# Kernel tuning notes

Hardware: AMD Instinct MI355X
Metric: run time of the kernel (lower is better)

Reference implementation:

```python
import jax, jax.numpy as jnp
import numpy as np

B = 1048576  # number of Gaussians
EPS = 1e-8


def setup_inputs() -> dict:
    key = jax.random.key(0)
    ks = jax.random.split(key, 6)
    return {
        "loc1": jax.random.normal(ks[0], (B, 3), dtype=jnp.float32),
        "scale1": jax.random.uniform(ks[1], (B, 3), dtype=jnp.float32),
        "rot_matrix1": jax.random.normal(ks[2], (B, 3, 3), dtype=jnp.float32),
        "loc2": jax.random.normal(ks[3], (B, 3), dtype=jnp.float32),
        "scale2": jax.random.uniform(ks[4], (B, 3), dtype=jnp.float32),
        "rot_matrix2": jax.random.normal(ks[5], (B, 3, 3), dtype=jnp.float32),
    }


def reference(loc1, scale1, rot_matrix1, loc2, scale2, rot_matrix2):
    # Wasserstein-2 distance between batched 3D Gaussians.
    scale1 = jnp.clip(scale1, EPS)
    scale2 = jnp.clip(scale2, EPS)

    loc_diff2 = jnp.sum((loc1 - loc2) ** 2, axis=-1)  # [B]

    # cov2 = R2 diag(scale2) R2^T  -> [B,3,3]
    cov2 = jnp.einsum('bij,bj,bkj->bik', rot_matrix2, scale2, rot_matrix2)

    # cov2 rotated into frame 1: R1^T cov2 R1
    cov2_R1 = jnp.einsum('bji,bjk,bkl->bil', rot_matrix1, cov2, rot_matrix1)

    # E = diag(sqrt(scale1)) cov2_R1 diag(sqrt(scale1)), symmetrized
    s1_sqrt = jnp.sqrt(scale1)  # [B,3]
    E = s1_sqrt[:, :, None] * cov2_R1 * s1_sqrt[:, None, :]
    E = 0.5 * (E + jnp.swapaxes(E, -1, -2)) + EPS * jnp.eye(3, dtype=E.dtype)

    eigs = jnp.clip(jnp.linalg.eigvalsh(E), EPS)  # [B,3]
    E_sqrt_trace = jnp.sqrt(eigs).sum(axis=-1)  # [B]

    cov_w = (scale1.sum(axis=-1)
             + jnp.einsum('bii->b', cov2)
             - 2.0 * E_sqrt_trace)
    cov_w = jnp.clip(cov_w, 0.0)

    return jnp.sqrt(jnp.clip(loc_diff2 + cov_w, EPS))
```

## Files before the change

### kernel.cpp

```cpp
#include <hip/hip_runtime.h>
#include <math.h>

#define EPSF 1e-8f

__device__ __forceinline__ float tr_sqrt_eig(double a00, double a11, double a22,
                                             double a01, double a02, double a12)
{
    double q = (a00 + a11 + a22) * (1.0 / 3.0);
    double b00 = a00 - q, b11 = a11 - q, b22 = a22 - q;
    double p1 = a01 * a01 + a02 * a02 + a12 * a12;
    double p2 = b00 * b00 + b11 * b11 + b22 * b22 + 2.0 * p1;

    if (p2 <= 1e-30) {
        return 3.0f * sqrtf(fmaxf((float)q, EPSF));
    }

    double x = p2 * (1.0 / 6.0);
    double inv = rsqrt(x);
    double p = x * inv;
    double detB = b00 * (b11 * b22 - a12 * a12)
                - a01 * (a01 * b22 - a12 * a02)
                + a02 * (a01 * a12 - b11 * a02);
    double r = 0.5 * detB * (inv * inv * inv);
    r = fmin(1.0, fmax(-1.0, r));

    float phi = acosf((float)r) * (1.0f / 3.0f);
    float qf = (float)q;
    float tp = 2.0f * (float)p;
    float e0 = qf + tp * cosf(phi);
    float e1 = qf + tp * cosf(phi - 2.0943951023931953f);
    float e2 = qf + tp * cosf(phi + 2.0943951023931953f);
    return sqrtf(fmaxf(e0, EPSF)) + sqrtf(fmaxf(e1, EPSF)) + sqrtf(fmaxf(e2, EPSF));
}

__global__ __launch_bounds__(64) void wasserstein_kernel(
    const float* __restrict__ loc1, const float* __restrict__ scale1,
    const float* __restrict__ rot1, const float* __restrict__ loc2,
    const float* __restrict__ scale2, const float* __restrict__ rot2,
    float* __restrict__ out, int B4)
{
    int t = blockIdx.x * blockDim.x + threadIdx.x;
    if (t >= B4) return;

    const float4* l1p = (const float4*)loc1   + 3 * t;
    const float4* l2p = (const float4*)loc2   + 3 * t;
    const float4* s1p = (const float4*)scale1 + 3 * t;
    const float4* s2p = (const float4*)scale2 + 3 * t;
    const float4* r1p = (const float4*)rot1   + 9 * t;
    const float4* r2p = (const float4*)rot2   + 9 * t;

    float loc_diff2[4];
    {
        float L1[12], L2[12];
#pragma unroll
        for (int k = 0; k < 3; k++) {
            float4 a = l1p[k], b = l2p[k];
            L1[4 * k + 0] = a.x; L1[4 * k + 1] = a.y; L1[4 * k + 2] = a.z; L1[4 * k + 3] = a.w;
            L2[4 * k + 0] = b.x; L2[4 * k + 1] = b.y; L2[4 * k + 2] = b.z; L2[4 * k + 3] = b.w;
        }
#pragma unroll
        for (int g = 0; g < 4; g++) {
            float d0 = L1[3 * g + 0] - L2[3 * g + 0];
            float d1 = L1[3 * g + 1] - L2[3 * g + 1];
            float d2 = L1[3 * g + 2] - L2[3 * g + 2];
            loc_diff2[g] = d0 * d0 + d1 * d1 + d2 * d2;
        }
    }

    float cov2[4][6];
    float tr_cov2[4];
    {
        float S2[12], R2[36];
#pragma unroll
        for (int k = 0; k < 3; k++) {
            float4 v = s2p[k];
            S2[4 * k + 0] = v.x; S2[4 * k + 1] = v.y; S2[4 * k + 2] = v.z; S2[4 * k + 3] = v.w;
        }
#pragma unroll
        for (int k = 0; k < 9; k++) {
            float4 v = r2p[k];
            R2[4 * k + 0] = v.x; R2[4 * k + 1] = v.y; R2[4 * k + 2] = v.z; R2[4 * k + 3] = v.w;
        }
#pragma unroll
        for (int g = 0; g < 4; g++) {
            float s0 = fmaxf(S2[3 * g + 0], EPSF);
            float s1 = fmaxf(S2[3 * g + 1], EPSF);
            float s2 = fmaxf(S2[3 * g + 2], EPSF);
            const float* R = R2 + 9 * g;
            float c00 = R[0] * s0 * R[0] + R[1] * s1 * R[1] + R[2] * s2 * R[2];
            float c11 = R[3] * s0 * R[3] + R[4] * s1 * R[4] + R[5] * s2 * R[5];
            float c22 = R[6] * s0 * R[6] + R[7] * s1 * R[7] + R[8] * s2 * R[8];
            float c01 = R[0] * s0 * R[3] + R[1] * s1 * R[4] + R[2] * s2 * R[5];
            float c02 = R[0] * s0 * R[6] + R[1] * s1 * R[7] + R[2] * s2 * R[8];
            float c12 = R[3] * s0 * R[6] + R[4] * s1 * R[7] + R[5] * s2 * R[8];
            cov2[g][0] = c00; cov2[g][1] = c11; cov2[g][2] = c22;
            cov2[g][3] = c01; cov2[g][4] = c02; cov2[g][5] = c12;
            tr_cov2[g] = c00 + c11 + c22;
        }
    }

    float res[4];
    {
        float S1[12], R1[36];
#pragma unroll
        for (int k = 0; k < 3; k++) {
            float4 v = s1p[k];
            S1[4 * k + 0] = v.x; S1[4 * k + 1] = v.y; S1[4 * k + 2] = v.z; S1[4 * k + 3] = v.w;
        }
#pragma unroll
        for (int k = 0; k < 9; k++) {
            float4 v = r1p[k];
            R1[4 * k + 0] = v.x; R1[4 * k + 1] = v.y; R1[4 * k + 2] = v.z; R1[4 * k + 3] = v.w;
        }
#pragma unroll
        for (int g = 0; g < 4; g++) {
            float s0 = fmaxf(S1[3 * g + 0], EPSF);
            float s1 = fmaxf(S1[3 * g + 1], EPSF);
            float s2 = fmaxf(S1[3 * g + 2], EPSF);
            const float* R = R1 + 9 * g;
            float C[3][3];
            C[0][0] = cov2[g][0]; C[1][1] = cov2[g][1]; C[2][2] = cov2[g][2];
            C[0][1] = C[1][0] = cov2[g][3];
            C[0][2] = C[2][0] = cov2[g][4];
            C[1][2] = C[2][1] = cov2[g][5];

            float T[3][3];
#pragma unroll
            for (int r = 0; r < 3; r++)
#pragma unroll
                for (int c = 0; c < 3; c++)
                    T[r][c] = C[r][0] * R[c] + C[r][1] * R[3 + c] + C[r][2] * R[6 + c];

            float M[3][3];
#pragma unroll
            for (int r = 0; r < 3; r++)
#pragma unroll
                for (int c = 0; c < 3; c++)
                    M[r][c] = R[r] * T[0][c] + R[3 + r] * T[1][c] + R[6 + r] * T[2][c];

            float ss0 = sqrtf(s0), ss1 = sqrtf(s1), ss2 = sqrtf(s2);
            double a00 = (double)(s0 * M[0][0]) + 1e-8;
            double a11 = (double)(s1 * M[1][1]) + 1e-8;
            double a22 = (double)(s2 * M[2][2]) + 1e-8;
            double a01 = (double)(0.5f * (M[0][1] + M[1][0]) * ss0 * ss1);
            double a02 = (double)(0.5f * (M[0][2] + M[2][0]) * ss0 * ss2);
            double a12 = (double)(0.5f * (M[1][2] + M[2][1]) * ss1 * ss2);

            float trs = tr_sqrt_eig(a00, a11, a22, a01, a02, a12);

            float cov_w = (s0 + s1 + s2) + tr_cov2[g] - 2.0f * trs;
            cov_w = fmaxf(cov_w, 0.0f);
            res[g] = sqrtf(fmaxf(loc_diff2[g] + cov_w, EPSF));
        }
    }

    float4 o;
    o.x = res[0]; o.y = res[1]; o.z = res[2]; o.w = res[3];
    ((float4*)out)[t] = o;
}

extern "C" void kernel_launch(void* const* d_in, const int* in_sizes, int n_in,
                              void* d_out, int out_size, void* d_ws, size_t ws_size,
                              hipStream_t stream) {
    const float* loc1   = (const float*)d_in[0];
    const float* scale1 = (const float*)d_in[1];
    const float* rot1   = (const float*)d_in[2];
    const float* loc2   = (const float*)d_in[3];
    const float* scale2 = (const float*)d_in[4];
    const float* rot2   = (const float*)d_in[5];
    float* out = (float*)d_out;

    int B = in_sizes[0] / 3;
    int B4 = B / 4;
    int block = 64;
    int grid = (B4 + block - 1) / block;
    wasserstein_kernel<<<grid, block, 0, stream>>>(loc1, scale1, rot1, loc2, scale2, rot2, out, B4);
}
```

Before: 160.5 us.

## Stage rotation matrices through LDS with coalesced loads, one Gaussian per thread

Switches from four Gaussians per thread with per-thread strided float4 loads to one Gaussian per thread in 256-thread blocks. The 3x3 rotation matrices are loaded cooperatively into shared memory with coalesced float4 accesses, then read back per thread. Locations and scales are read directly with scalar strided loads. This aims to improve global-memory coalescing and occupancy, at the cost of a block barrier, LDS traffic with stride-9 access, and no bounds check, which assumes B is a multiple of 256.

```diff
diff --git a/kernel.cpp b/kernel.cpp
--- a/kernel.cpp
+++ b/kernel.cpp
@@ -33,130 +33,93 @@
     return sqrtf(fmaxf(e0, EPSF)) + sqrtf(fmaxf(e1, EPSF)) + sqrtf(fmaxf(e2, EPSF));
 }
 
-__global__ __launch_bounds__(64) void wasserstein_kernel(
+__global__ __launch_bounds__(256) void wasserstein_kernel(
     const float* __restrict__ loc1, const float* __restrict__ scale1,
     const float* __restrict__ rot1, const float* __restrict__ loc2,
     const float* __restrict__ scale2, const float* __restrict__ rot2,
-    float* __restrict__ out, int B4)
+    float* __restrict__ out, int B)
 {
-    int t = blockIdx.x * blockDim.x + threadIdx.x;
-    if (t >= B4) return;
+    __shared__ float sR1[256 * 9];
+    __shared__ float sR2[256 * 9];
 
-    const float4* l1p = (const float4*)loc1   + 3 * t;
-    const float4* l2p = (const float4*)loc2   + 3 * t;
-    const float4* s1p = (const float4*)scale1 + 3 * t;
-    const float4* s2p = (const float4*)scale2 + 3 * t;
-    const float4* r1p = (const float4*)rot1   + 9 * t;
-    const float4* r2p = (const float4*)rot2   + 9 * t;
+    const int tid = threadIdx.x;
+    const int g = blockIdx.x * 256 + tid;
 
-    float loc_diff2[4];
     {
-        float L1[12], L2[12];
-#pragma unroll
-        for (int k = 0; k < 3; k++) {
-            float4 a = l1p[k], b = l2p[k];
-            L1[4 * k + 0] = a.x; L1[4 * k + 1] = a.y; L1[4 * k + 2] = a.z; L1[4 * k + 3] = a.w;
-            L2[4 * k + 0] = b.x; L2[4 * k + 1] = b.y; L2[4 * k + 2] = b.z; L2[4 * k + 3] = b.w;
-        }
-#pragma unroll
-        for (int g = 0; g < 4; g++) {
-            float d0 = L1[3 * g + 0] - L2[3 * g + 0];
-            float d1 = L1[3 * g + 1] - L2[3 * g + 1];
-            float d2 = L1[3 * g + 2] - L2[3 * g + 2];
-            loc_diff2[g] = d0 * d0 + d1 * d1 + d2 * d2;
+        const float4* r1g = (const float4*)rot1 + blockIdx.x * 576;
+        const float4* r2g = (const float4*)rot2 + blockIdx.x * 576;
+        float4* s1 = (float4*)sR1;
+        float4* s2 = (float4*)sR2;
+        s1[tid]       = r1g[tid];
+        s1[tid + 256] = r1g[tid + 256];
+        s2[tid]       = r2g[tid];
+        s2[tid + 256] = r2g[tid + 256];
+        if (tid < 64) {
+            s1[tid + 512] = r1g[tid + 512];
+            s2[tid + 512] = r2g[tid + 512];
         }
     }
 
-    float cov2[4][6];
-    float tr_cov2[4];
-    {
-        float S2[12], R2[36];
+    float a0 = loc1[3 * g], a1 = loc1[3 * g + 1], a2 = loc1[3 * g + 2];
+    float b0 = loc2[3 * g], b1 = loc2[3 * g + 1], b2 = loc2[3 * g + 2];
+    float s10 = fmaxf(scale1[3 * g], EPSF);
+    float s11 = fmaxf(scale1[3 * g + 1], EPSF);
+    float s12 = fmaxf(scale1[3 * g + 2], EPSF);
+    float s20 = fmaxf(scale2[3 * g], EPSF);
+    float s21 = fmaxf(scale2[3 * g + 1], EPSF);
+    float s22 = fmaxf(scale2[3 * g + 2], EPSF);
+
+    float d0 = a0 - b0, d1 = a1 - b1, d2 = a2 - b2;
+    float loc_diff2 = d0 * d0 + d1 * d1 + d2 * d2;
+
+    __syncthreads();
+
+    const float* R2 = sR2 + 9 * tid;
+    float R2r[9];
 #pragma unroll
-        for (int k = 0; k < 3; k++) {
-            float4 v = s2p[k];
-            S2[4 * k + 0] = v.x; S2[4 * k + 1] = v.y; S2[4 * k + 2] = v.z; S2[4 * k + 3] = v.w;
-        }
+    for (int k = 0; k < 9; k++) R2r[k] = R2[k];
+
+    float C[3][3];
+    C[0][0] = R2r[0] * s20 * R2r[0] + R2r[1] * s21 * R2r[1] + R2r[2] * s22 * R2r[2];
+    C[1][1] = R2r[3] * s20 * R2r[3] + R2r[4] * s21 * R2r[4] + R2r[5] * s22 * R2r[5];
+    C[2][2] = R2r[6] * s20 * R2r[6] + R2r[7] * s21 * R2r[7] + R2r[8] * s22 * R2r[8];
+    C[0][1] = C[1][0] = R2r[0] * s20 * R2r[3] + R2r[1] * s21 * R2r[4] + R2r[2] * s22 * R2r[5];
+    C[0][2] = C[2][0] = R2r[0] * s20 * R2r[6] + R2r[1] * s21 * R2r[7] + R2r[2] * s22 * R2r[8];
+    C[1][2] = C[2][1] = R2r[3] * s20 * R2r[6] + R2r[4] * s21 * R2r[7] + R2r[5] * s22 * R2r[8];
+    float tr_cov2 = C[0][0] + C[1][1] + C[2][2];
+
+    const float* R1 = sR1 + 9 * tid;
+    float R1r[9];
 #pragma unroll
-        for (int k = 0; k < 9; k++) {
-            float4 v = r2p[k];
-            R2[4 * k + 0] = v.x; R2[4 * k + 1] = v.y; R2[4 * k + 2] = v.z; R2[4 * k + 3] = v.w;
-        }
+    for (int k = 0; k < 9; k++) R1r[k] = R1[k];
+
+    float T[3][3];
 #pragma unroll
-        for (int g = 0; g < 4; g++) {
-            float s0 = fmaxf(S2[3 * g + 0], EPSF);
-            float s1 = fmaxf(S2[3 * g + 1], EPSF);
-            float s2 = fmaxf(S2[3 * g + 2], EPSF);
-            const float* R = R2 + 9 * g;
-            float c00 = R[0] * s0 * R[0] + R[1] * s1 * R[1] + R[2] * s2 * R[2];
-            float c11 = R[3] * s0 * R[3] + R[4] * s1 * R[4] + R[5] * s2 * R[5];
-            float c22 = R[6] * s0 * R[6] + R[7] * s1 * R[7] + R[8] * s2 * R[8];
-            float c01 = R[0] * s0 * R[3] + R[1] * s1 * R[4] + R[2] * s2 * R[5];
-            float c02 = R[0] * s0 * R[6] + R[1] * s1 * R[7] + R[2] * s2 * R[8];
-            float c12 = R[3] * s0 * R[6] + R[4] * s1 * R[7] + R[5] * s2 * R[8];
-            cov2[g][0] = c00; cov2[g][1] = c11; cov2[g][2] = c22;
-            cov2[g][3] = c01; cov2[g][4] = c02; cov2[g][5] = c12;
-            tr_cov2[g] = c00 + c11 + c22;
-        }
-    }
+    for (int r = 0; r < 3; r++)
+#pragma unroll
+        for (int c = 0; c < 3; c++)
+            T[r][c] = C[r][0] * R1r[c] + C[r][1] * R1r[3 + c] + C[r][2] * R1r[6 + c];
 
-    float res[4];
-    {
-        float S1[12], R1[36];
+    float M[3][3];
 #pragma unroll
-        for (int k = 0; k < 3; k++) {
-            float4 v = s1p[k];
-            S1[4 * k + 0] = v.x; S1[4 * k + 1] = v.y; S1[4 * k + 2] = v.z; S1[4 * k + 3] = v.w;
-        }
+    for (int r = 0; r < 3; r++)
 #pragma unroll
-        for (int k = 0; k < 9; k++) {
-            float4 v = r1p[k];
-            R1[4 * k + 0] = v.x; R1[4 * k + 1] = v.y; R1[4 * k + 2] = v.z; R1[4 * k + 3] = v.w;
-        }
-#pragma unroll
-        for (int g = 0; g < 4; g++) {
-            float s0 = fmaxf(S1[3 * g + 0], EPSF);
-            float s1 = fmaxf(S1[3 * g + 1], EPSF);
-            float s2 = fmaxf(S1[3 * g + 2], EPSF);
-            const float* R = R1 + 9 * g;
-            float C[3][3];
-            C[0][0] = cov2[g][0]; C[1][1] = cov2[g][1]; C[2][2] = cov2[g][2];
-            C[0][1] = C[1][0] = cov2[g][3];
-            C[0][2] = C[2][0] = cov2[g][4];
-            C[1][2] = C[2][1] = cov2[g][5];
+        for (int c = 0; c < 3; c++)
+            M[r][c] = R1r[r] * T[0][c] + R1r[3 + r] * T[1][c] + R1r[6 + r] * T[2][c];
 
-            float T[3][3];
-#pragma unroll
-            for (int r = 0; r < 3; r++)
-#pragma unroll
-                for (int c = 0; c < 3; c++)
-                    T[r][c] = C[r][0] * R[c] + C[r][1] * R[3 + c] + C[r][2] * R[6 + c];
+    float ss0 = sqrtf(s10), ss1 = sqrtf(s11), ss2 = sqrtf(s12);
+    double a00 = (double)(s10 * M[0][0]) + 1e-8;
+    double a11 = (double)(s11 * M[1][1]) + 1e-8;
+    double a22 = (double)(s12 * M[2][2]) + 1e-8;
+    double a01 = (double)(0.5f * (M[0][1] + M[1][0]) * ss0 * ss1);
+    double a02 = (double)(0.5f * (M[0][2] + M[2][0]) * ss0 * ss2);
+    double a12 = (double)(0.5f * (M[1][2] + M[2][1]) * ss1 * ss2);
 
-            float M[3][3];
-#pragma unroll
-            for (int r = 0; r < 3; r++)
-#pragma unroll
-                for (int c = 0; c < 3; c++)
-                    M[r][c] = R[r] * T[0][c] + R[3 + r] * T[1][c] + R[6 + r] * T[2][c];
+    float trs = tr_sqrt_eig(a00, a11, a22, a01, a02, a12);
 
-            float ss0 = sqrtf(s0), ss1 = sqrtf(s1), ss2 = sqrtf(s2);
-            double a00 = (double)(s0 * M[0][0]) + 1e-8;
-            double a11 = (double)(s1 * M[1][1]) + 1e-8;
-            double a22 = (double)(s2 * M[2][2]) + 1e-8;
-            double a01 = (double)(0.5f * (M[0][1] + M[1][0]) * ss0 * ss1);
-            double a02 = (double)(0.5f * (M[0][2] + M[2][0]) * ss0 * ss2);
-            double a12 = (double)(0.5f * (M[1][2] + M[2][1]) * ss1 * ss2);
-
-            float trs = tr_sqrt_eig(a00, a11, a22, a01, a02, a12);
-
-            float cov_w = (s0 + s1 + s2) + tr_cov2[g] - 2.0f * trs;
-            cov_w = fmaxf(cov_w, 0.0f);
-            res[g] = sqrtf(fmaxf(loc_diff2[g] + cov_w, EPSF));
-        }
-    }
-
-    float4 o;
-    o.x = res[0]; o.y = res[1]; o.z = res[2]; o.w = res[3];
-    ((float4*)out)[t] = o;
+    float cov_w = (s10 + s11 + s12) + tr_cov2 - 2.0f * trs;
+    cov_w = fmaxf(cov_w, 0.0f);
+    out[g] = sqrtf(fmaxf(loc_diff2 + cov_w, EPSF));
 }
 
 extern "C" void kernel_launch(void* const* d_in, const int* in_sizes, int n_in,
@@ -171,8 +134,6 @@
     float* out = (float*)d_out;
 
     int B = in_sizes[0] / 3;
-    int B4 = B / 4;
-    int block = 64;
-    int grid = (B4 + block - 1) / block;
-    wasserstein_kernel<<<grid, block, 0, stream>>>(loc1, scale1, rot1, loc2, scale2, rot2, out, B4);
+    int grid = B / 256;
+    wasserstein_kernel<<<grid, 256, 0, stream>>>(loc1, scale1, rot1, loc2, scale2, rot2, out, B);
 }
```

Result: faster. 147.3 us (-8.2%).
